# Kernel tuning notes

Measured on AMD Instinct MI355X. Metric: run time of the kernel, lower is better.

Reference implementation:

```python
import jax, jax.numpy as jnp
import numpy as np

DIM_IN, HID, N = 3, 512, 65536


def _xavier(key, shape):
    fan_in, fan_out = shape[1], shape[0]
    lim = np.sqrt(6.0 / (fan_in + fan_out))
    return jax.random.uniform(key, shape, jnp.float32, -lim, lim)


def setup_inputs() -> dict:
    key = jax.random.key(0)
    names_shapes = [
        ("W1", (HID, DIM_IN)), ("b1", (HID, 1)),
        ("Uz1", (HID, DIM_IN)), ("Wz1", (HID, HID)), ("bz1", (HID, 1)),
        ("Ug1", (HID, DIM_IN)), ("Wg1", (HID, HID)), ("bg1", (HID, 1)),
        ("Ur1", (HID, DIM_IN)), ("Wr1", (HID, HID)), ("br1", (HID, 1)),
        ("Uh1", (HID, DIM_IN)), ("Wh1", (HID, HID)), ("bh1", (HID, 1)),
        ("Uz2", (HID, DIM_IN)), ("Wz2", (HID, HID)), ("bz2", (HID, 1)),
        ("Ug2", (HID, DIM_IN)), ("Wg2", (HID, HID)), ("bg2", (HID, 1)),
        ("Ur2", (HID, DIM_IN)), ("Wr2", (HID, HID)), ("br2", (HID, 1)),
        ("Uh2", (HID, DIM_IN)), ("Wh2", (HID, HID)), ("bh2", (HID, 1)),
        ("W", (1, HID)), ("b", (1, 1)),
    ]
    keys = jax.random.split(key, len(names_shapes) + 1)
    inp = {"x": jax.random.normal(keys[0], (DIM_IN, N), jnp.float32)}
    for k, (nm, sh) in zip(keys[1:], names_shapes):
        inp[nm] = _xavier(k, sh)
    return inp


def reference(x, W1, b1, Uz1, Wz1, bz1, Ug1, Wg1, bg1, Ur1, Wr1, br1,
              Uh1, Wh1, bh1, Uz2, Wz2, bz2, Ug2, Wg2, bg2, Ur2, Wr2, br2,
              Uh2, Wh2, bh2, W, b):
    # x: (dim_in, N); all hidden states are (hidden_sz, N)
    S1 = jnp.tanh(W1 @ x + b1)
    Z1 = jnp.tanh(Uz1 @ x + Wz1 @ S1 + bz1)
    G1 = jnp.tanh(Ug1 @ x + Wg1 @ S1 + bg1)
    R1 = jnp.tanh(Ur1 @ x + Wr1 @ S1 + br1)
    H1 = jnp.tanh(Uh1 @ x + Wh1 @ (S1 * R1) + bh1)
    S2 = (1.0 - G1) * H1 + Z1 * S1
    Z2 = jnp.tanh(Uz2 @ x + Wz2 @ S2 + bz2)
    G2 = jnp.tanh(Ug2 @ x + Wg2 @ S2 + bg2)
    R2 = jnp.tanh(Ur2 @ x + Wr2 @ S2 + br2)
    H2 = jnp.tanh(Uh2 @ x + Wh2 @ (S2 * R2) + bh2)
    S3 = (1.0 - G2) * H2 + Z2 * S2
    return W @ S3 + b  # (1, N)
```

## Files before the change

kernel.cpp:

```cpp
#include <hip/hip_runtime.h>

typedef unsigned short u16;
typedef unsigned int   u32;
typedef short bf16x8 __attribute__((ext_vector_type(8)));
typedef float f32x4  __attribute__((ext_vector_type(4)));
typedef unsigned short u16x4 __attribute__((ext_vector_type(4)));
typedef unsigned int   u32x2 __attribute__((ext_vector_type(2)));

#define HID   512
#define NT    64
#define NCOL  65536
#define PADC  520
#define MAT_ELEMS (512 * 512)

__device__ __forceinline__ float bf2f(u16 v) {
  union { u32 u; float f; } t; t.u = ((u32)v) << 16; return t.f;
}
__device__ __forceinline__ u16 f2bf(float f) {
  union { float f; u32 u; } t; t.f = f;
  u32 r = t.u + 0x7fffu + ((t.u >> 16) & 1u);
  return (u16)(r >> 16);
}
__device__ __forceinline__ float lo16(u32 v) { return bf2f((u16)(v & 0xffffu)); }
__device__ __forceinline__ float hi16(u32 v) { return bf2f((u16)(v >> 16)); }
__device__ __forceinline__ u32 pk2(float lo, float hi) {
  u32 r;
  asm("v_cvt_pk_bf16_f32 %0, %1, %2" : "=v"(r) : "v"(lo), "v"(hi));
  return r;
}
__device__ __forceinline__ float ldv(const void* p, int i, int isbf) {
  return isbf ? bf2f(((const u16*)p)[i]) : ((const float*)p)[i];
}
__device__ __forceinline__ float tanh_fast(float x) {
  float e = __builtin_amdgcn_exp2f(x * 2.8853900817779268f);
  return 1.0f - 2.0f * __builtin_amdgcn_rcpf(e + 1.0f);
}

__global__ void sniff_kernel(const u16* x, u32* flag) {
  if (threadIdx.x == 0 && blockIdx.x == 0) {
    int cnt = 0;
    for (int i = 0; i < 256; i++) {
      u32 e = (x[i] >> 7) & 0xFFu;
      if (e == 0u || (e >= 100u && e <= 140u)) cnt++;
    }
    *flag = (cnt >= 220) ? 1u : 0u;
  }
}

struct PrepArgs {
  const void* U[9]; const void* B[9];
  const void* Wout; const void* bout;
  float* dst; const u32* flag;
};

__global__ void prep_kernel(PrepArgs a) {
  int t = blockIdx.x * 256 + threadIdx.x;
  const int isbf = (int)*a.flag;
  if (t < 9 * 512) {
    int m = t >> 9, r = t & 511;
    float4 v;
    v.x = ldv(a.U[m], r * 3 + 0, isbf);
    v.y = ldv(a.U[m], r * 3 + 1, isbf);
    v.z = ldv(a.U[m], r * 3 + 2, isbf);
    v.w = ldv(a.B[m], r, isbf);
    ((float4*)a.dst)[t] = v;
  } else if (t < 9 * 512 + 512) {
    int r = t - 9 * 512;
    a.dst[9 * 2048 + r] = ldv(a.Wout, r, isbf);
    if (r == 0) a.dst[9 * 2048 + 512] = ldv(a.bout, 0, isbf);
  }
}

struct SwzArgs { const void* src[8]; u16* dst; const u32* flag; };

__global__ void swizzle_kernel(SwzArgs a) {
  const int isbf = (int)*a.flag;
  int t = blockIdx.x * 256 + threadIdx.x;
  int m    = t >> 15;
  int rem  = t & 32767;
  int tile = rem >> 6;
  int lane = rem & 63;
  int kb = tile >> 5, rt = tile & 31;
  int row = rt * 16 + (lane & 15);
  int k   = kb * 32 + (lane >> 4) * 8;
  u16 tmp[8];
  if (isbf) {
    const u16* s = (const u16*)a.src[m] + row * 512 + k;
#pragma unroll
    for (int j = 0; j < 8; j++) tmp[j] = s[j];
  } else {
    const float* s = (const float*)a.src[m] + row * 512 + k;
#pragma unroll
    for (int j = 0; j < 8; j++) tmp[j] = f2bf(s[j]);
  }
  uint4* d = (uint4*)(a.dst + (size_t)m * MAT_ELEMS + (size_t)tile * 512 + lane * 8);
  *d = *(const uint4*)tmp;
}

struct KArgs {
  const void* x;
  const u16* ws;
  const float4* ub;
  const u32* flag;
  void* out;
};

__device__ __forceinline__ void init_acc(f32x4 acc[4][2],
    const float4* __restrict__ ub, const float xv[2][3], int rowslab, int quad)
{
#pragma unroll
  for (int rt = 0; rt < 4; rt++) {
#pragma unroll
    for (int i = 0; i < 4; i++) {
      int r = rowslab * 64 + rt * 16 + quad * 4 + i;
      float4 u = ub[r];
#pragma unroll
      for (int ct = 0; ct < 2; ct++)
        acc[rt][ct][i] = u.x * xv[ct][0] + u.y * xv[ct][1] + u.z * xv[ct][2] + u.w;
    }
  }
}

__device__ __forceinline__ void gemm64(f32x4 acc[4][2],
    const u16* __restrict__ wmat, const u16* ldsB, int rowslab, int wc,
    int lane, int l15, int quad)
{
  const u16* abase = wmat + (size_t)(rowslab * 4) * 512 + lane * 8;
  const u16* bbase = ldsB + (wc * 32 + l15) * PADC + quad * 8;
#pragma unroll
  for (int kb = 0; kb < 16; kb++) {
    bf16x8 b[2];
#pragma unroll
    for (int ct = 0; ct < 2; ct++)
      b[ct] = *(const bf16x8*)(bbase + kb * 32 + ct * 16 * PADC);
    bf16x8 a[4];
#pragma unroll
    for (int i = 0; i < 4; i++)
      a[i] = *(const bf16x8*)(abase + (size_t)kb * 32 * 512 + i * 512);
    __builtin_amdgcn_s_setprio(1);
#pragma unroll
    for (int rt = 0; rt < 4; rt++)
#pragma unroll
      for (int ct = 0; ct < 2; ct++)
        acc[rt][ct] = __builtin_amdgcn_mfma_f32_16x16x32_bf16(a[rt], b[ct], acc[rt][ct], 0, 0, 0);
    __builtin_amdgcn_s_setprio(0);
  }
}

__global__ __launch_bounds__(1024, 4) void pdenet_kernel(KArgs ka) {
  __shared__ __align__(16) u16 ldsS[NT * PADC];
  __shared__ __align__(16) u16 ldsR[NT * PADC];
  __shared__ float xs[3 * NT];

  const int isbf = (int)*ka.flag;
  const int tid  = threadIdx.x;
  const int wave = tid >> 6;
  const int rowslab = wave >> 1;
  const int wc   = wave & 1;
  const int lane = tid & 63;
  const int l15  = lane & 15;
  const int quad = lane >> 4;
  const int c0   = blockIdx.x * NT;

  if (tid < 3 * NT)
    xs[tid] = ldv(ka.x, (tid >> 6) * NCOL + c0 + (tid & 63), isbf);
  __syncthreads();

  {
    int r  = tid & 511;
    int ch = tid >> 9;
    float4 w = ka.ub[8 * 512 + r];
#pragma unroll 4
    for (int cc = 0; cc < 32; cc++) {
      int c = ch * 32 + cc;
      float s = tanh_fast(w.x * xs[c] + w.y * xs[NT + c] + w.z * xs[2 * NT + c] + w.w);
      ldsS[c * PADC + r] = f2bf(s);
    }
  }

  float xv[2][3];
#pragma unroll
  for (int ct = 0; ct < 2; ct++) {
    int c = wc * 32 + ct * 16 + l15;
    xv[ct][0] = xs[c]; xv[ct][1] = xs[NT + c]; xv[ct][2] = xs[2 * NT + c];
  }
  __syncthreads();

  u32 zpk[4][2][2], opk[4][2][2];

#pragma unroll
  for (int layer = 0; layer < 2; layer++) {
    const int g0 = layer * 4;

    {
      f32x4 acc[4][2];
      init_acc(acc, ka.ub + (size_t)(g0 + 0) * 512, xv, rowslab, quad);
      gemm64(acc, ka.ws + (size_t)(g0 + 0) * MAT_ELEMS, ldsS, rowslab, wc, lane, l15, quad);
#pragma unroll
      for (int rt = 0; rt < 4; rt++)
#pragma unroll
        for (int ct = 0; ct < 2; ct++) {
          zpk[rt][ct][0] = pk2(tanh_fast(acc[rt][ct][0]), tanh_fast(acc[rt][ct][1]));
          zpk[rt][ct][1] = pk2(tanh_fast(acc[rt][ct][2]), tanh_fast(acc[rt][ct][3]));
        }
    }
    {
      f32x4 acc[4][2];
      init_acc(acc, ka.ub + (size_t)(g0 + 1) * 512, xv, rowslab, quad);
      gemm64(acc, ka.ws + (size_t)(g0 + 1) * MAT_ELEMS, ldsS, rowslab, wc, lane, l15, quad);
#pragma unroll
      for (int rt = 0; rt < 4; rt++)
#pragma unroll
        for (int ct = 0; ct < 2; ct++) {
          opk[rt][ct][0] = pk2(1.0f - tanh_fast(acc[rt][ct][0]),
                               1.0f - tanh_fast(acc[rt][ct][1]));
          opk[rt][ct][1] = pk2(1.0f - tanh_fast(acc[rt][ct][2]),
                               1.0f - tanh_fast(acc[rt][ct][3]));
        }
    }
    {
      f32x4 acc[4][2];
      init_acc(acc, ka.ub + (size_t)(g0 + 2) * 512, xv, rowslab, quad);
      gemm64(acc, ka.ws + (size_t)(g0 + 2) * MAT_ELEMS, ldsS, rowslab, wc, lane, l15, quad);
#pragma unroll
      for (int rt = 0; rt < 4; rt++)
#pragma unroll
        for (int ct = 0; ct < 2; ct++) {
          int c  = wc * 32 + ct * 16 + l15;
          int rb = rowslab * 64 + rt * 16 + quad * 4;
          u16x4 sv4 = *(const u16x4*)&ldsS[c * PADC + rb];
          float sv0 = bf2f(sv4[0]), sv1 = bf2f(sv4[1]);
          float sv2 = bf2f(sv4[2]), sv3 = bf2f(sv4[3]);
          u32x2 sr;
          sr[0] = pk2(sv0 * tanh_fast(acc[rt][ct][0]), sv1 * tanh_fast(acc[rt][ct][1]));
          sr[1] = pk2(sv2 * tanh_fast(acc[rt][ct][2]), sv3 * tanh_fast(acc[rt][ct][3]));
          u32 zp0 = zpk[rt][ct][0], zp1 = zpk[rt][ct][1];
          zpk[rt][ct][0] = pk2(lo16(zp0) * sv0, hi16(zp0) * sv1);
          zpk[rt][ct][1] = pk2(lo16(zp1) * sv2, hi16(zp1) * sv3);
          *(u32x2*)&ldsR[c * PADC + rb] = sr;
        }
    }
    __syncthreads();
    {
      f32x4 acc[4][2];
      init_acc(acc, ka.ub + (size_t)(g0 + 3) * 512, xv, rowslab, quad);
      gemm64(acc, ka.ws + (size_t)(g0 + 3) * MAT_ELEMS, ldsR, rowslab, wc, lane, l15, quad);
#pragma unroll
      for (int rt = 0; rt < 4; rt++)
#pragma unroll
        for (int ct = 0; ct < 2; ct++) {
          int c  = wc * 32 + ct * 16 + l15;
          int rb = rowslab * 64 + rt * 16 + quad * 4;
          u32 zp0 = zpk[rt][ct][0], zp1 = zpk[rt][ct][1];
          u32 op0 = opk[rt][ct][0], op1 = opk[rt][ct][1];
          u32x2 sn;
          sn[0] = pk2(lo16(op0) * tanh_fast(acc[rt][ct][0]) + lo16(zp0),
                      hi16(op0) * tanh_fast(acc[rt][ct][1]) + hi16(zp0));
          sn[1] = pk2(lo16(op1) * tanh_fast(acc[rt][ct][2]) + lo16(zp1),
                      hi16(op1) * tanh_fast(acc[rt][ct][3]) + hi16(zp1));
          *(u32x2*)&ldsS[c * PADC + rb] = sn;
        }
    }
    __syncthreads();
  }

  {
    int c   = tid >> 4;
    int seg = tid & 15;
    const u16* s3 = &ldsS[c * PADC + seg * 32];
    const float* wv = (const float*)(ka.ub + 9 * 512);
    const float4* w4 = (const float4*)(wv + seg * 32);
    float p = 0.0f;
#pragma unroll
    for (int j = 0; j < 8; j++) {
      u16x4 sv = *(const u16x4*)&s3[j * 4];
      float4 w = w4[j];
      p += w.x * bf2f(sv[0]) + w.y * bf2f(sv[1]) + w.z * bf2f(sv[2]) + w.w * bf2f(sv[3]);
    }
    p += __shfl_xor(p, 1);
    p += __shfl_xor(p, 2);
    p += __shfl_xor(p, 4);
    p += __shfl_xor(p, 8);
    if (seg == 0) {
      float res = p + wv[512];
      if (isbf) ((u16*)ka.out)[c0 + c] = f2bf(res);
      else      ((float*)ka.out)[c0 + c] = res;
    }
  }
}

extern "C" void kernel_launch(void* const* d_in, const int* in_sizes, int n_in,
                              void* d_out, int out_size, void* d_ws, size_t ws_size,
                              hipStream_t stream) {
  static const int widx[8] = {4, 7, 10, 13, 16, 19, 22, 25};
  static const int uidx[8] = {3, 6, 9, 12, 15, 18, 21, 24};
  static const int bidx[8] = {5, 8, 11, 14, 17, 20, 23, 26};

  u16*   ws16  = (u16*)d_ws;
  u32*   flagp = (u32*)((char*)d_ws + (size_t)8 * MAT_ELEMS * 2);
  float* ubp   = (float*)((char*)d_ws + (size_t)8 * MAT_ELEMS * 2 + 16);

  hipLaunchKernelGGL(sniff_kernel, dim3(1), dim3(64), 0, stream,
                     (const u16*)d_in[0], flagp);

  PrepArgs pa;
  for (int i = 0; i < 8; i++) { pa.U[i] = d_in[uidx[i]]; pa.B[i] = d_in[bidx[i]]; }
  pa.U[8] = d_in[1]; pa.B[8] = d_in[2];
  pa.Wout = d_in[27]; pa.bout = d_in[28];
  pa.dst = ubp; pa.flag = flagp;
  hipLaunchKernelGGL(prep_kernel, dim3(20), dim3(256), 0, stream, pa);

  SwzArgs sa;
  for (int i = 0; i < 8; i++) sa.src[i] = d_in[widx[i]];
  sa.dst  = ws16;
  sa.flag = flagp;
  hipLaunchKernelGGL(swizzle_kernel, dim3(1024), dim3(256), 0, stream, sa);

  KArgs ka;
  ka.x    = d_in[0];
  ka.ws   = ws16;
  ka.ub   = (const float4*)ubp;
  ka.flag = flagp;
  ka.out  = d_out;
  hipLaunchKernelGGL(pdenet_kernel, dim3(NCOL / NT), dim3(1024), 0, stream, ka);
}
```

Before: 482.5 us.

## Fold input projection and bias into GEMM as an extra K tile

Adds a 17th K tile to each swizzled weight matrix holding the U columns and bias, and appends x values plus a constant one to the LDS activation buffers. Accumulators then start at zero instead of being set by a scalar FMA pass over the U/bias table. This removes the per-gate init_acc loads and VALU work but adds about 6% more MFMA and weight traffic, widens the LDS row padding, and rounds x and the bias to bf16.

```diff
diff --git a/kernel.cpp b/kernel.cpp
--- a/kernel.cpp
+++ b/kernel.cpp
@@ -10,8 +10,10 @@
 #define HID   512
 #define NT    64
 #define NCOL  65536
-#define PADC  520
-#define MAT_ELEMS (512 * 512)
+#define KTILES 17
+#define KEXT  544
+#define PADC  584
+#define WMAT_ELEMS (KTILES * 32 * 512)
 
 __device__ __forceinline__ float bf2f(u16 v) {
   union { u32 u; float f; } t; t.u = ((u32)v) << 16; return t.f;
@@ -71,29 +73,46 @@
   }
 }
 
-struct SwzArgs { const void* src[8]; u16* dst; const u32* flag; };
+struct SwzArgs {
+  const void* src[8];
+  const void* usrc[8];
+  const void* bsrc[8];
+  u16* dst; const u32* flag;
+};
 
 __global__ void swizzle_kernel(SwzArgs a) {
   const int isbf = (int)*a.flag;
   int t = blockIdx.x * 256 + threadIdx.x;
-  int m    = t >> 15;
-  int rem  = t & 32767;
+  int m    = t / (KTILES * 32 * 64);
+  int rem  = t - m * (KTILES * 32 * 64);
   int tile = rem >> 6;
   int lane = rem & 63;
   int kb = tile >> 5, rt = tile & 31;
   int row = rt * 16 + (lane & 15);
-  int k   = kb * 32 + (lane >> 4) * 8;
+  int kk  = (lane >> 4) * 8;
   u16 tmp[8];
-  if (isbf) {
-    const u16* s = (const u16*)a.src[m] + row * 512 + k;
-#pragma unroll
-    for (int j = 0; j < 8; j++) tmp[j] = s[j];
+  if (kb < 16) {
+    int k = kb * 32 + kk;
+    if (isbf) {
+      const u16* s = (const u16*)a.src[m] + row * 512 + k;
+#pragma unroll
+      for (int j = 0; j < 8; j++) tmp[j] = s[j];
+    } else {
+      const float* s = (const float*)a.src[m] + row * 512 + k;
+#pragma unroll
+      for (int j = 0; j < 8; j++) tmp[j] = f2bf(s[j]);
+    }
   } else {
-    const float* s = (const float*)a.src[m] + row * 512 + k;
-#pragma unroll
-    for (int j = 0; j < 8; j++) tmp[j] = f2bf(s[j]);
-  }
-  uint4* d = (uint4*)(a.dst + (size_t)m * MAT_ELEMS + (size_t)tile * 512 + lane * 8);
+#pragma unroll
+    for (int j = 0; j < 8; j++) {
+      int kidx = kk + j;
+      float v = (kidx < 3) ? ldv(a.usrc[m], row * 3 + kidx, isbf)
+              : (kidx == 3) ? ldv(a.bsrc[m], row, isbf)
+              : 0.0f;
+      tmp[j] = f2bf(v);
+    }
+  }
+  uint4* d = (uint4*)(a.dst + (size_t)m * WMAT_ELEMS + (size_t)tile * 512 + lane * 8);
   *d = *(const uint4*)tmp;
 }
 
@@ -105,22 +124,6 @@
   void* out;
 };
 
-__device__ __forceinline__ void init_acc(f32x4 acc[4][2],
-    const float4* __restrict__ ub, const float xv[2][3], int rowslab, int quad)
-{
-#pragma unroll
-  for (int rt = 0; rt < 4; rt++) {
-#pragma unroll
-    for (int i = 0; i < 4; i++) {
-      int r = rowslab * 64 + rt * 16 + quad * 4 + i;
-      float4 u = ub[r];
-#pragma unroll
-      for (int ct = 0; ct < 2; ct++)
-        acc[rt][ct][i] = u.x * xv[ct][0] + u.y * xv[ct][1] + u.z * xv[ct][2] + u.w;
-    }
-  }
-}
-
 __device__ __forceinline__ void gemm64(f32x4 acc[4][2],
     const u16* __restrict__ wmat, const u16* ldsB, int rowslab, int wc,
     int lane, int l15, int quad)
@@ -128,7 +131,7 @@
   const u16* abase = wmat + (size_t)(rowslab * 4) * 512 + lane * 8;
   const u16* bbase = ldsB + (wc * 32 + l15) * PADC + quad * 8;
 #pragma unroll
-  for (int kb = 0; kb < 16; kb++) {
+  for (int kb = 0; kb < KTILES; kb++) {
     bf16x8 b[2];
 #pragma unroll
     for (int ct = 0; ct < 2; ct++)
@@ -178,11 +181,17 @@
     }
   }
 
-  float xv[2][3];
-#pragma unroll
-  for (int ct = 0; ct < 2; ct++) {
-    int c = wc * 32 + ct * 16 + l15;
-    xv[ct][0] = xs[c]; xv[ct][1] = xs[NT + c]; xv[ct][2] = xs[2 * NT + c];
+  {
+#pragma unroll
+    for (int rep = 0; rep < 2; rep++) {
+      int e = tid + rep * 1024;
+      int c = e >> 5, j = e & 31;
+      float v = (j == 0) ? xs[c] : (j == 1) ? xs[NT + c]
+              : (j == 2) ? xs[2 * NT + c] : (j == 3) ? 1.0f : 0.0f;
+      u16 bv = f2bf(v);
+      ldsS[c * PADC + 512 + j] = bv;
+      ldsR[c * PADC + 512 + j] = bv;
+    }
   }
   __syncthreads();
 
@@ -193,9 +202,8 @@
     const int g0 = layer * 4;
 
     {
-      f32x4 acc[4][2];
-      init_acc(acc, ka.ub + (size_t)(g0 + 0) * 512, xv, rowslab, quad);
-      gemm64(acc, ka.ws + (size_t)(g0 + 0) * MAT_ELEMS, ldsS, rowslab, wc, lane, l15, quad);
+      f32x4 acc[4][2] = {};
+      gemm64(acc, ka.ws + (size_t)(g0 + 0) * WMAT_ELEMS, ldsS, rowslab, wc, lane, l15, quad);
 #pragma unroll
       for (int rt = 0; rt < 4; rt++)
 #pragma unroll
@@ -205,9 +213,8 @@
         }
     }
     {
-      f32x4 acc[4][2];
-      init_acc(acc, ka.ub + (size_t)(g0 + 1) * 512, xv, rowslab, quad);
-      gemm64(acc, ka.ws + (size_t)(g0 + 1) * MAT_ELEMS, ldsS, rowslab, wc, lane, l15, quad);
+      f32x4 acc[4][2] = {};
+      gemm64(acc, ka.ws + (size_t)(g0 + 1) * WMAT_ELEMS, ldsS, rowslab, wc, lane, l15, quad);
 #pragma unroll
       for (int rt = 0; rt < 4; rt++)
 #pragma unroll
@@ -219,9 +226,8 @@
         }
     }
     {
-      f32x4 acc[4][2];
-      init_acc(acc, ka.ub + (size_t)(g0 + 2) * 512, xv, rowslab, quad);
-      gemm64(acc, ka.ws + (size_t)(g0 + 2) * MAT_ELEMS, ldsS, rowslab, wc, lane, l15, quad);
+      f32x4 acc[4][2] = {};
+      gemm64(acc, ka.ws + (size_t)(g0 + 2) * WMAT_ELEMS, ldsS, rowslab, wc, lane, l15, quad);
 #pragma unroll
       for (int rt = 0; rt < 4; rt++)
 #pragma unroll
@@ -242,9 +248,8 @@
     }
     __syncthreads();
     {
-      f32x4 acc[4][2];
-      init_acc(acc, ka.ub + (size_t)(g0 + 3) * 512, xv, rowslab, quad);
-      gemm64(acc, ka.ws + (size_t)(g0 + 3) * MAT_ELEMS, ldsR, rowslab, wc, lane, l15, quad);
+      f32x4 acc[4][2] = {};
+      gemm64(acc, ka.ws + (size_t)(g0 + 3) * WMAT_ELEMS, ldsR, rowslab, wc, lane, l15, quad);
 #pragma unroll
       for (int rt = 0; rt < 4; rt++)
 #pragma unroll
@@ -297,8 +302,8 @@
   static const int bidx[8] = {5, 8, 11, 14, 17, 20, 23, 26};
 
   u16*   ws16  = (u16*)d_ws;
-  u32*   flagp = (u32*)((char*)d_ws + (size_t)8 * MAT_ELEMS * 2);
-  float* ubp   = (float*)((char*)d_ws + (size_t)8 * MAT_ELEMS * 2 + 16);
+  u32*   flagp = (u32*)((char*)d_ws + (size_t)8 * WMAT_ELEMS * 2);
+  float* ubp   = (float*)((char*)d_ws + (size_t)8 * WMAT_ELEMS * 2 + 16);
 
   hipLaunchKernelGGL(sniff_kernel, dim3(1), dim3(64), 0, stream,
                      (const u16*)d_in[0], flagp);
@@ -311,10 +316,14 @@
   hipLaunchKernelGGL(prep_kernel, dim3(20), dim3(256), 0, stream, pa);
 
   SwzArgs sa;
-  for (int i = 0; i < 8; i++) sa.src[i] = d_in[widx[i]];
+  for (int i = 0; i < 8; i++) {
+    sa.src[i]  = d_in[widx[i]];
+    sa.usrc[i] = d_in[uidx[i]];
+    sa.bsrc[i] = d_in[bidx[i]];
+  }
   sa.dst  = ws16;
   sa.flag = flagp;
-  hipLaunchKernelGGL(swizzle_kernel, dim3(1024), dim3(256), 0, stream, sa);
+  hipLaunchKernelGGL(swizzle_kernel, dim3(1088), dim3(256), 0, stream, sa);
 
   KArgs ka;
   ka.x    = d_in[0];
```

Result: faster. 454.4 us (-5.8%).
